# Optimization experiments

Hardware: AMD Instinct MI355X
Metric: run time of the kernel (lower is better)

The kernel has to match this reference:

```python
import jax, jax.numpy as jnp
import numpy as np

N = 100000      # nodes
E = 1600000     # edges (avg degree 16)
F_IN = 128
F_OUT = 128
EPS = 1e-5      # BatchNorm eps


def setup_inputs() -> dict:
    key = jax.random.key(0)
    ks = jax.random.split(key, 10)
    s_in = 1.0 / np.sqrt(F_IN)
    s_out = 1.0 / np.sqrt(F_OUT)
    return {
        "x": jax.random.normal(ks[0], (N, F_IN), dtype=jnp.float32),
        "edge_index": jax.random.randint(ks[1], (2, E), 0, N, dtype=jnp.int32),
        # layer 0: SAGEConv(F_IN, F_OUT, aggr='max'); lin_l has bias, lin_r does not
        "W0_l": jax.random.normal(ks[2], (F_IN, F_OUT), dtype=jnp.float32) * s_in,
        "b0_l": jnp.zeros((F_OUT,), dtype=jnp.float32),
        "W0_r": jax.random.normal(ks[3], (F_IN, F_OUT), dtype=jnp.float32) * s_in,
        "gamma0": jnp.ones((F_OUT,), dtype=jnp.float32),
        "beta0": jnp.zeros((F_OUT,), dtype=jnp.float32),
        # layer 1: SAGEConv(F_OUT, F_OUT, aggr='max')
        "W1_l": jax.random.normal(ks[4], (F_OUT, F_OUT), dtype=jnp.float32) * s_out,
        "b1_l": jnp.zeros((F_OUT,), dtype=jnp.float32),
        "W1_r": jax.random.normal(ks[5], (F_OUT, F_OUT), dtype=jnp.float32) * s_out,
        "gamma1": jnp.ones((F_OUT,), dtype=jnp.float32),
        "beta1": jnp.zeros((F_OUT,), dtype=jnp.float32),
    }


def _sage_conv_max(x, src, dst, W_l, b_l, W_r):
    # gather source features along edges, scatter-max into destination nodes
    msgs = x[src]                                             # [E, F]
    agg = jax.ops.segment_max(msgs, dst, num_segments=N)      # [N, F], -inf for isolated
    agg = jnp.where(jnp.isfinite(agg), agg, 0.0)              # PyG fills empty segments with 0
    return agg @ W_l + b_l + x @ W_r                          # lin_l(aggr) + lin_r(x)


def _batch_norm(h, gamma, beta):
    mu = jnp.mean(h, axis=0)
    var = jnp.var(h, axis=0)
    return (h - mu) * jax.lax.rsqrt(var + EPS) * gamma + beta


def reference(x, edge_index, W0_l, b0_l, W0_r, gamma0, beta0,
              W1_l, b1_l, W1_r, gamma1, beta1):
    src, dst = edge_index[0], edge_index[1]
    h = _sage_conv_max(x, src, dst, W0_l, b0_l, W0_r)
    h = jax.nn.relu(_batch_norm(h, gamma0, beta0))
    h = _sage_conv_max(h, src, dst, W1_l, b1_l, W1_r)
    h = jax.nn.relu(_batch_norm(h, gamma1, beta1))
    return h
```

## Files before the change

### kernel.cpp

```cpp
#include <hip/hip_runtime.h>
#include <stdint.h>

#define EPS_BN 1e-5f

typedef __attribute__((ext_vector_type(8))) short short8v;
typedef __attribute__((ext_vector_type(4))) float f32x4;

__device__ __forceinline__ unsigned rne_bf16(float f) {
    unsigned u = __float_as_uint(f);
    return (u + 0x7FFFu + ((u >> 16) & 1u)) >> 16;
}

extern "C" __global__ __launch_bounds__(256)
void f32_to_bf16_kernel(const float4* __restrict__ in, uint2* __restrict__ out, long n4) {
    long i = (long)blockIdx.x * 256 + threadIdx.x;
    long stride = (long)gridDim.x * 256;
    for (; i < n4; i += stride) {
        float4 v = in[i];
        uint2 o;
        o.x = rne_bf16(v.x) | (rne_bf16(v.y) << 16);
        o.y = rne_bf16(v.z) | (rne_bf16(v.w) << 16);
        out[i] = o;
    }
}

extern "C" __global__ __launch_bounds__(256)
void wt_prep_kernel(const float* __restrict__ Wl, const float* __restrict__ Wr,
                    unsigned short* __restrict__ Wt) {
    int idx = blockIdx.x * 256 + threadIdx.x;
    int col = idx >> 8, k = idx & 255;
    float v = (k < 128) ? Wl[(size_t)k * 128 + col] : Wr[(size_t)(k - 128) * 128 + col];
    Wt[(size_t)col * 256 + k] = (unsigned short)rne_bf16(v);
}

extern "C" __global__ __launch_bounds__(256)
void init_head_kernel(int* __restrict__ head, int n) {
    int i = blockIdx.x * 256 + threadIdx.x;
    if (i < n) head[i] = -1;
}

extern "C" __global__ __launch_bounds__(256)
void link_kernel(const int* __restrict__ ei, int* __restrict__ head,
                 int* __restrict__ next, int E) {
    int e = blockIdx.x * 256 + threadIdx.x;
    if (e < E) {
        int dst = ei[E + e];
        int old = atomicExch(&head[dst], e);
        next[e] = old;
    }
}

extern "C" __global__ __launch_bounds__(256)
void gather_max_ll16_kernel(const uint2* __restrict__ x16, const int* __restrict__ head,
                            const int* __restrict__ next, const int* __restrict__ ei,
                            uint2* __restrict__ agg16, int Nn) {
    int t = blockIdx.x * 256 + threadIdx.x;
    int node = t >> 5;
    if (node >= Nn) return;
    int lane = t & 31;
    int e = head[node];
    uint2 out;
    if (e >= 0) {
        int src = ei[e];
        int en = next[e];
        uint2 u = x16[(size_t)src * 32 + lane];
        float a0 = __uint_as_float(u.x << 16);
        float a1 = __uint_as_float(u.x & 0xFFFF0000u);
        float a2 = __uint_as_float(u.y << 16);
        float a3 = __uint_as_float(u.y & 0xFFFF0000u);
        while (en >= 0) {
            int s2 = ei[en];
            int en2 = next[en];
            uint2 v = x16[(size_t)s2 * 32 + lane];
            en = en2;
            a0 = fmaxf(a0, __uint_as_float(v.x << 16));
            a1 = fmaxf(a1, __uint_as_float(v.x & 0xFFFF0000u));
            a2 = fmaxf(a2, __uint_as_float(v.y << 16));
            a3 = fmaxf(a3, __uint_as_float(v.y & 0xFFFF0000u));
        }
        out.x = (__float_as_uint(a0) >> 16) | (__float_as_uint(a1) & 0xFFFF0000u);
        out.y = (__float_as_uint(a2) >> 16) | (__float_as_uint(a3) & 0xFFFF0000u);
    } else {
        out.x = 0u; out.y = 0u;
    }
    agg16[(size_t)node * 32 + lane] = out;
}

extern "C" __global__ __launch_bounds__(256)
void gemm_bf16_kernel(const unsigned short* __restrict__ agg16,
                      const unsigned short* __restrict__ xin16,
                      const unsigned short* __restrict__ Wt,
                      const float* __restrict__ bias,
                      float* __restrict__ h, float* __restrict__ stats, int nrows) {
    __shared__ float redS[4][128];
    __shared__ float redQ[4][128];

    const int t = threadIdx.x;
    const int w = t >> 6, l = t & 63;
    const int wm = w >> 1, wn = w & 1;
    const int r16 = l & 15, g = l >> 4;
    const int blockRow = blockIdx.x * 128;
    const int colBase = wn * 64;

    f32x4 acc[4][4];
#pragma unroll
    for (int m = 0; m < 4; ++m)
#pragma unroll
        for (int n = 0; n < 4; ++n) acc[m][n] = (f32x4){0.f, 0.f, 0.f, 0.f};

    const short8v az = {0, 0, 0, 0, 0, 0, 0, 0};

#pragma unroll
    for (int kt = 0; kt < 8; ++kt) {
        const unsigned short* Asrc = (kt < 4) ? agg16 : xin16;
        const int kofs = (kt < 4) ? kt * 32 : kt * 32 - 128;

        short8v b[4];
#pragma unroll
        for (int n = 0; n < 4; ++n) {
            int col = colBase + n * 16 + r16;
            b[n] = *(const short8v*)(Wt + (size_t)col * 256 + kt * 32 + g * 8);
        }
        short8v a[4];
#pragma unroll
        for (int m = 0; m < 4; ++m) {
            int row = blockRow + wm * 64 + m * 16 + r16;
            a[m] = (row < nrows)
                 ? *(const short8v*)(Asrc + (size_t)row * 128 + kofs + g * 8)
                 : az;
        }
#pragma unroll
        for (int m = 0; m < 4; ++m)
#pragma unroll
            for (int n = 0; n < 4; ++n)
                acc[m][n] = __builtin_amdgcn_mfma_f32_16x16x32_bf16(a[m], b[n], acc[m][n], 0, 0, 0);
    }

    for (int i = t; i < 512; i += 256) {
        ((float*)redS)[i] = 0.f;
        ((float*)redQ)[i] = 0.f;
    }
    __syncthreads();

    float bcol[4];
#pragma unroll
    for (int n = 0; n < 4; ++n) bcol[n] = bias[colBase + n * 16 + r16];

    float s4[4] = {0.f, 0.f, 0.f, 0.f};
    float q4[4] = {0.f, 0.f, 0.f, 0.f};
#pragma unroll
    for (int m = 0; m < 4; ++m) {
#pragma unroll
        for (int reg = 0; reg < 4; ++reg) {
            int row = blockRow + wm * 64 + m * 16 + g * 4 + reg;
            if (row < nrows) {
#pragma unroll
                for (int n = 0; n < 4; ++n) {
                    float o = acc[m][n][reg] + bcol[n];
                    h[(size_t)row * 128 + colBase + n * 16 + r16] = o;
                    s4[n] += o;
                    q4[n] += o * o;
                }
            }
        }
    }
#pragma unroll
    for (int n = 0; n < 4; ++n) {
        s4[n] += __shfl_xor(s4[n], 16, 64);
        s4[n] += __shfl_xor(s4[n], 32, 64);
        q4[n] += __shfl_xor(q4[n], 16, 64);
        q4[n] += __shfl_xor(q4[n], 32, 64);
    }
    if (g == 0) {
#pragma unroll
        for (int n = 0; n < 4; ++n) {
            redS[w][colBase + n * 16 + r16] = s4[n];
            redQ[w][colBase + n * 16 + r16] = q4[n];
        }
    }
    __syncthreads();
    if (t < 128) {
        float s = redS[0][t] + redS[1][t] + redS[2][t] + redS[3][t];
        float q = redQ[0][t] + redQ[1][t] + redQ[2][t] + redQ[3][t];
        atomicAdd(&stats[t], s);
        atomicAdd(&stats[128 + t], q);
    }
}

extern "C" __global__
void zero_stats_kernel(float* __restrict__ stats) {
    stats[threadIdx.x] = 0.0f;
}

extern "C" __global__
void finalize_kernel(const float* __restrict__ stats, const float* __restrict__ gamma,
                     const float* __restrict__ beta, float* __restrict__ ss, float inv_n) {
    int c = threadIdx.x;
    if (c < 128) {
        float mu = stats[c] * inv_n;
        float var = stats[128 + c] * inv_n - mu * mu;
        float sc = gamma[c] * rsqrtf(var + EPS_BN);
        ss[c] = sc;
        ss[128 + c] = beta[c] - mu * sc;
    }
}

extern "C" __global__ __launch_bounds__(256)
void bn_relu_tobf16_kernel(const float4* __restrict__ h, const float* __restrict__ ss,
                           uint2* __restrict__ y16, long n4) {
    __shared__ float s_ss[256];
    if (threadIdx.x < 256) s_ss[threadIdx.x] = ss[threadIdx.x];
    __syncthreads();
    long i = (long)blockIdx.x * blockDim.x + threadIdx.x;
    long stride = (long)gridDim.x * blockDim.x;
    for (; i < n4; i += stride) {
        int c4 = (int)(i & 31) * 4;
        float4 v = h[i];
        float o0 = fmaxf(fmaf(v.x, s_ss[c4 + 0], s_ss[128 + c4 + 0]), 0.f);
        float o1 = fmaxf(fmaf(v.y, s_ss[c4 + 1], s_ss[128 + c4 + 1]), 0.f);
        float o2 = fmaxf(fmaf(v.z, s_ss[c4 + 2], s_ss[128 + c4 + 2]), 0.f);
        float o3 = fmaxf(fmaf(v.w, s_ss[c4 + 3], s_ss[128 + c4 + 3]), 0.f);
        uint2 o;
        o.x = rne_bf16(o0) | (rne_bf16(o1) << 16);
        o.y = rne_bf16(o2) | (rne_bf16(o3) << 16);
        y16[i] = o;
    }
}

extern "C" __global__ __launch_bounds__(256)
void bn_relu_kernel(float4* __restrict__ h, const float* __restrict__ ss, long n4) {
    __shared__ float s_ss[256];
    if (threadIdx.x < 256) s_ss[threadIdx.x] = ss[threadIdx.x];
    __syncthreads();
    long i = (long)blockIdx.x * blockDim.x + threadIdx.x;
    long stride = (long)gridDim.x * blockDim.x;
    for (; i < n4; i += stride) {
        int c4 = (int)(i & 31) * 4;
        float4 v = h[i];
        v.x = fmaxf(fmaf(v.x, s_ss[c4 + 0], s_ss[128 + c4 + 0]), 0.f);
        v.y = fmaxf(fmaf(v.y, s_ss[c4 + 1], s_ss[128 + c4 + 1]), 0.f);
        v.z = fmaxf(fmaf(v.z, s_ss[c4 + 2], s_ss[128 + c4 + 2]), 0.f);
        v.w = fmaxf(fmaf(v.w, s_ss[c4 + 3], s_ss[128 + c4 + 3]), 0.f);
        h[i] = v;
    }
}

__device__ __forceinline__ unsigned map_f(float f) {
    unsigned u = __float_as_uint(f);
    return (u & 0x80000000u) ? ~u : (u | 0x80000000u);
}
__device__ __forceinline__ float unmap_f(unsigned m) {
    return (m & 0x80000000u) ? __uint_as_float(m & 0x7FFFFFFFu) : __uint_as_float(~m);
}

extern "C" __global__ __launch_bounds__(256)
void init_sentinel_kernel(uint4* __restrict__ agg, long n4) {
    uint4 z = {0u, 0u, 0u, 0u};
    long i = (long)blockIdx.x * blockDim.x + threadIdx.x;
    long stride = (long)gridDim.x * blockDim.x;
    for (; i < n4; i += stride) agg[i] = z;
}

extern "C" __global__ __launch_bounds__(256)
void scatter_max_kernel(const float4* __restrict__ xin, const int* __restrict__ ei,
                        unsigned* __restrict__ agg, int E) {
    int t = blockIdx.x * 256 + threadIdx.x;
    int e = t >> 5;
    if (e >= E) return;
    int f4 = t & 31;
    int src = ei[e];
    int dst = ei[E + e];
    float4 v = xin[(size_t)src * 32 + f4];
    unsigned* p = agg + (size_t)dst * 128 + (size_t)f4 * 4;
    atomicMax(p + 0, map_f(v.x));
    atomicMax(p + 1, map_f(v.y));
    atomicMax(p + 2, map_f(v.z));
    atomicMax(p + 3, map_f(v.w));
}

extern "C" __global__ __launch_bounds__(256)
void unmap_kernel(unsigned* __restrict__ agg, long n) {
    long i = (long)blockIdx.x * blockDim.x + threadIdx.x;
    long stride = (long)gridDim.x * blockDim.x;
    for (; i < n; i += stride) {
        unsigned u = agg[i];
        agg[i] = __float_as_uint(u ? unmap_f(u) : 0.0f);
    }
}

extern "C" __global__ __launch_bounds__(256)
void gemm_kernel(const float* __restrict__ agg, const float* __restrict__ xin,
                 const float* __restrict__ Wl, const float* __restrict__ Wr,
                 const float* __restrict__ bias, float* __restrict__ h,
                 float* __restrict__ stats, int nrows) {
    __shared__ __align__(16) float As[64][36];
    __shared__ __align__(16) float Bs[32][136];
    __shared__ float redS[4][128];
    __shared__ float redQ[4][128];

    const int t = threadIdx.x;
    const int tx = t & 15;
    const int ty = t >> 4;
    const int tx8 = tx * 8;
    const int ty4 = ty * 4;
    const int blockRow = blockIdx.x * 64;

    float acc[4][8];
#pragma unroll
    for (int j = 0; j < 4; ++j)
#pragma unroll
        for (int c = 0; c < 8; ++c) acc[j][c] = 0.0f;

    for (int kt = 0; kt < 8; ++kt) {
        const int k0 = kt * 32;
        const bool isAgg = (kt < 4);
        const float* W = isAgg ? Wl : Wr;
        const float* Asrc = isAgg ? agg : xin;
        const int kw = isAgg ? k0 : (k0 - 128);

#pragma unroll
        for (int it = 0; it < 4; ++it) {
            int idx = t + it * 256;
            int kr = idx >> 5, cq = idx & 31;
            float4 ww = *(const float4*)&W[(size_t)(kw + kr) * 128 + cq * 4];
            *(float4*)&Bs[kr][cq * 4] = ww;
        }
#pragma unroll
        for (int it = 0; it < 2; ++it) {
            int idx = t + it * 256;
            int r = idx >> 3, kq = idx & 7;
            int row_g = blockRow + r;
            float4 a = {0.f, 0.f, 0.f, 0.f};
            if (row_g < nrows)
                a = *(const float4*)&Asrc[(size_t)row_g * 128 + kw + kq * 4];
            *(float4*)&As[r][kq * 4] = a;
        }
        __syncthreads();

#pragma unroll
        for (int kk = 0; kk < 32; ++kk) {
            float aa[4];
            aa[0] = As[ty4 + 0][kk];
            aa[1] = As[ty4 + 1][kk];
            aa[2] = As[ty4 + 2][kk];
            aa[3] = As[ty4 + 3][kk];
            float4 b0 = *(const float4*)&Bs[kk][tx8];
            float4 b1 = *(const float4*)&Bs[kk][tx8 + 4];
            float bb[8] = {b0.x, b0.y, b0.z, b0.w, b1.x, b1.y, b1.z, b1.w};
#pragma unroll
            for (int j = 0; j < 4; ++j)
#pragma unroll
                for (int c = 0; c < 8; ++c)
                    acc[j][c] = fmaf(aa[j], bb[c], acc[j][c]);
        }
        __syncthreads();
    }

    float bv[8];
#pragma unroll
    for (int c = 0; c < 8; ++c) bv[c] = bias[tx8 + c];

    float s_loc[8], q_loc[8];
#pragma unroll
    for (int c = 0; c < 8; ++c) { s_loc[c] = 0.f; q_loc[c] = 0.f; }

#pragma unroll
    for (int j = 0; j < 4; ++j) {
        int row = blockRow + ty4 + j;
        if (row < nrows) {
            float o[8];
#pragma unroll
            for (int c = 0; c < 8; ++c) {
                o[c] = acc[j][c] + bv[c];
                s_loc[c] += o[c];
                q_loc[c] += o[c] * o[c];
            }
            float4 o0 = {o[0], o[1], o[2], o[3]};
            float4 o1 = {o[4], o[5], o[6], o[7]};
            *(float4*)&h[(size_t)row * 128 + tx8] = o0;
            *(float4*)&h[(size_t)row * 128 + tx8 + 4] = o1;
        }
    }

#pragma unroll
    for (int c = 0; c < 8; ++c) {
        s_loc[c] += __shfl_xor(s_loc[c], 16, 64);
        s_loc[c] += __shfl_xor(s_loc[c], 32, 64);
        q_loc[c] += __shfl_xor(q_loc[c], 16, 64);
        q_loc[c] += __shfl_xor(q_loc[c], 32, 64);
    }
    int wave = t >> 6;
    if ((t & 63) < 16) {
#pragma unroll
        for (int c = 0; c < 8; ++c) {
            redS[wave][tx8 + c] = s_loc[c];
            redQ[wave][tx8 + c] = q_loc[c];
        }
    }
    __syncthreads();
    if (t < 128) {
        float s = redS[0][t] + redS[1][t] + redS[2][t] + redS[3][t];
        float q = redQ[0][t] + redQ[1][t] + redQ[2][t] + redQ[3][t];
        atomicAdd(&stats[t], s);
        atomicAdd(&stats[128 + t], q);
    }
}

static void run_layer_bf16(const unsigned short* in16, const int* head, const int* next,
                           const int* ei, int Nn,
                           const unsigned short* Wt, const float* bl,
                           const float* gamma, const float* beta,
                           unsigned short* agg16, float* stats, float* ss,
                           float* h, hipStream_t stream) {
    zero_stats_kernel<<<1, 256, 0, stream>>>(stats);
    gather_max_ll16_kernel<<<(Nn * 32 + 255) / 256, 256, 0, stream>>>(
        (const uint2*)in16, head, next, ei, (uint2*)agg16, Nn);
    gemm_bf16_kernel<<<(Nn + 127) / 128, 256, 0, stream>>>(agg16, in16, Wt, bl,
                                                           h, stats, Nn);
    finalize_kernel<<<1, 128, 0, stream>>>(stats, gamma, beta, ss, 1.0f / (float)Nn);
}

static void run_layer_atomic(const float* in_feat, const int* ei, int Nn, int Ee,
                             const float* Wl, const float* bl, const float* Wr,
                             const float* gamma, const float* beta,
                             float* agg, float* stats, float* ss,
                             float* out, hipStream_t stream) {
    long aggN = (long)Nn * 128;
    long n4 = aggN / 4;

    zero_stats_kernel<<<1, 256, 0, stream>>>(stats);
    int initBlocks = (int)((n4 + 255) / 256);
    if (initBlocks > 4096) initBlocks = 4096;
    init_sentinel_kernel<<<initBlocks, 256, 0, stream>>>((uint4*)agg, n4);
    int sb = (int)(((long)Ee * 32 + 255) / 256);
    scatter_max_kernel<<<sb, 256, 0, stream>>>((const float4*)in_feat, ei,
                                               (unsigned*)agg, Ee);
    int ub = (int)((aggN + 255) / 256);
    if (ub > 8192) ub = 8192;
    unmap_kernel<<<ub, 256, 0, stream>>>((unsigned*)agg, aggN);
    gemm_kernel<<<(Nn + 63) / 64, 256, 0, stream>>>(agg, in_feat, Wl, Wr, bl,
                                                    out, stats, Nn);
    finalize_kernel<<<1, 128, 0, stream>>>(stats, gamma, beta, ss, 1.0f / (float)Nn);
    int bnBlocks = (int)((n4 + 255) / 256);
    if (bnBlocks > 8192) bnBlocks = 8192;
    bn_relu_kernel<<<bnBlocks, 256, 0, stream>>>((float4*)out, ss, n4);
}

extern "C" void kernel_launch(void* const* d_in, const int* in_sizes, int n_in,
                              void* d_out, int out_size, void* d_ws, size_t ws_size,
                              hipStream_t stream) {
    (void)n_in; (void)out_size;
    const float* x     = (const float*)d_in[0];
    const int*   ei    = (const int*)d_in[1];
    const float* W0_l  = (const float*)d_in[2];
    const float* b0_l  = (const float*)d_in[3];
    const float* W0_r  = (const float*)d_in[4];
    const float* g0    = (const float*)d_in[5];
    const float* be0   = (const float*)d_in[6];
    const float* W1_l  = (const float*)d_in[7];
    const float* b1_l  = (const float*)d_in[8];
    const float* W1_r  = (const float*)d_in[9];
    const float* g1    = (const float*)d_in[10];
    const float* be1   = (const float*)d_in[11];

    int Nn = in_sizes[0] / 128;
    int Ee = in_sizes[1] / 2;
    long n4 = (long)Nn * 32;

    char* p = (char*)d_ws;
    unsigned short* xy16 = (unsigned short*)p;  p += (size_t)Nn * 128 * 2;
    unsigned short* agg16 = (unsigned short*)p; p += (size_t)Nn * 128 * 2;
    float* stats = (float*)p;                   p += 256 * sizeof(float);
    float* ss = (float*)p;                      p += 256 * sizeof(float);
    unsigned short* Wt0 = (unsigned short*)p;   p += 128 * 256 * 2;
    unsigned short* Wt1 = (unsigned short*)p;   p += 128 * 256 * 2;
    int* head = (int*)p;                        p += (size_t)Nn * sizeof(int);
    int* next = (int*)p;                        p += (size_t)Ee * sizeof(int);
    size_t needed = (size_t)(p - (char*)d_ws);
    float* out = (float*)d_out;

    if (ws_size >= needed) {
        int cvB = (int)((n4 + 255) / 256);
        if (cvB > 4096) cvB = 4096;
        f32_to_bf16_kernel<<<cvB, 256, 0, stream>>>((const float4*)x, (uint2*)xy16, n4);
        wt_prep_kernel<<<128, 256, 0, stream>>>(W0_l, W0_r, Wt0);
        wt_prep_kernel<<<128, 256, 0, stream>>>(W1_l, W1_r, Wt1);
        init_head_kernel<<<(Nn + 255) / 256, 256, 0, stream>>>(head, Nn);
        link_kernel<<<(Ee + 255) / 256, 256, 0, stream>>>(ei, head, next, Ee);

        run_layer_bf16(xy16, head, next, ei, Nn, Wt0, b0_l, g0, be0,
                       agg16, stats, ss, out, stream);
        int bnB = (int)((n4 + 255) / 256);
        if (bnB > 8192) bnB = 8192;
        bn_relu_tobf16_kernel<<<bnB, 256, 0, stream>>>((const float4*)out, ss,
                                                       (uint2*)xy16, n4);
        run_layer_bf16(xy16, head, next, ei, Nn, Wt1, b1_l, g1, be1,
                       agg16, stats, ss, out, stream);
        bn_relu_kernel<<<bnB, 256, 0, stream>>>((float4*)out, ss, n4);
    } else {
        float* agg = (float*)d_ws;
        float* fstats = (float*)((char*)d_ws + (size_t)Nn * 128 * sizeof(float));
        float* fss = fstats + 256;
        run_layer_atomic(x, ei, Nn, Ee, W0_l, b0_l, W0_r, g0, be0,
                         agg, fstats, fss, out, stream);
        run_layer_atomic(out, ei, Nn, Ee, W1_l, b1_l, W1_r, g1, be1,
                         agg, fstats, fss, out, stream);
    }
}
```

Baseline: 464.0 us.

## Pack src/next edge pairs, widen gather to 16B per lane, fuse stats zeroing

```diff
diff --git a/kernel.cpp b/kernel.cpp
--- a/kernel.cpp
+++ b/kernel.cpp
@@ -41,49 +41,57 @@
 
 extern "C" __global__ __launch_bounds__(256)
 void link_kernel(const int* __restrict__ ei, int* __restrict__ head,
-                 int* __restrict__ next, int E) {
+                 uint2* __restrict__ pair, int E) {
     int e = blockIdx.x * 256 + threadIdx.x;
     if (e < E) {
+        int src = ei[e];
         int dst = ei[E + e];
         int old = atomicExch(&head[dst], e);
-        next[e] = old;
-    }
-}
-
-extern "C" __global__ __launch_bounds__(256)
-void gather_max_ll16_kernel(const uint2* __restrict__ x16, const int* __restrict__ head,
-                            const int* __restrict__ next, const int* __restrict__ ei,
-                            uint2* __restrict__ agg16, int Nn) {
+        uint2 p; p.x = (unsigned)src; p.y = (unsigned)old;
+        pair[e] = p;
+    }
+}
+
+extern "C" __global__ __launch_bounds__(256, 8)
+void gather_max_ll16_kernel(const uint4* __restrict__ x16r, const int* __restrict__ head,
+                            const uint2* __restrict__ pair,
+                            uint4* __restrict__ agg16, float* __restrict__ stats, int Nn) {
+    if (blockIdx.x == 0 && threadIdx.x < 256) stats[threadIdx.x] = 0.0f;
     int t = blockIdx.x * 256 + threadIdx.x;
-    int node = t >> 5;
+    int node = t >> 4;
     if (node >= Nn) return;
-    int lane = t & 31;
+    int lane = t & 15;
     int e = head[node];
-    uint2 out;
+    uint4 out;
     if (e >= 0) {
-        int src = ei[e];
-        int en = next[e];
-        uint2 u = x16[(size_t)src * 32 + lane];
-        float a0 = __uint_as_float(u.x << 16);
-        float a1 = __uint_as_float(u.x & 0xFFFF0000u);
-        float a2 = __uint_as_float(u.y << 16);
-        float a3 = __uint_as_float(u.y & 0xFFFF0000u);
+        uint2 p = pair[e];
+        uint4 r = x16r[(size_t)p.x * 16 + lane];
+        float a0 = __uint_as_float(r.x << 16), a1 = __uint_as_float(r.x);
+        float a2 = __uint_as_float(r.y << 16), a3 = __uint_as_float(r.y);
+        float a4 = __uint_as_float(r.z << 16), a5 = __uint_as_float(r.z);
+        float a6 = __uint_as_float(r.w << 16), a7 = __uint_as_float(r.w);
+        int en = (int)p.y;
         while (en >= 0) {
-            int s2 = ei[en];
-            int en2 = next[en];
-            uint2 v = x16[(size_t)s2 * 32 + lane];
-            en = en2;
+            uint2 pn = pair[en];
+            uint4 v = x16r[(size_t)pn.x * 16 + lane];
+            en = (int)pn.y;
             a0 = fmaxf(a0, __uint_as_float(v.x << 16));
-            a1 = fmaxf(a1, __uint_as_float(v.x & 0xFFFF0000u));
+            a1 = fmaxf(a1, __uint_as_float(v.x));
             a2 = fmaxf(a2, __uint_as_float(v.y << 16));
-            a3 = fmaxf(a3, __uint_as_float(v.y & 0xFFFF0000u));
+            a3 = fmaxf(a3, __uint_as_float(v.y));
+            a4 = fmaxf(a4, __uint_as_float(v.z << 16));
+            a5 = fmaxf(a5, __uint_as_float(v.z));
+            a6 = fmaxf(a6, __uint_as_float(v.w << 16));
+            a7 = fmaxf(a7, __uint_as_float(v.w));
         }
         out.x = (__float_as_uint(a0) >> 16) | (__float_as_uint(a1) & 0xFFFF0000u);
         out.y = (__float_as_uint(a2) >> 16) | (__float_as_uint(a3) & 0xFFFF0000u);
+        out.z = (__float_as_uint(a4) >> 16) | (__float_as_uint(a5) & 0xFFFF0000u);
+        out.w = (__float_as_uint(a6) >> 16) | (__float_as_uint(a7) & 0xFFFF0000u);
     } else {
-        out.x = 0u; out.y = 0u;
-    }
-    agg16[(size_t)node * 32 + lane] = out;
+        out.x = out.y = out.z = out.w = 0u;
+    }
+    agg16[(size_t)node * 16 + lane] = out;
 }
 
 extern "C" __global__ __launch_bounds__(256)
@@ -406,15 +414,13 @@
     }
 }
 
-static void run_layer_bf16(const unsigned short* in16, const int* head, const int* next,
-                           const int* ei, int Nn,
-                           const unsigned short* Wt, const float* bl,
+static void run_layer_bf16(const unsigned short* in16, const int* head, const uint2* pair,
+                           int Nn, const unsigned short* Wt, const float* bl,
                            const float* gamma, const float* beta,
                            unsigned short* agg16, float* stats, float* ss,
                            float* h, hipStream_t stream) {
-    zero_stats_kernel<<<1, 256, 0, stream>>>(stats);
-    gather_max_ll16_kernel<<<(Nn * 32 + 255) / 256, 256, 0, stream>>>(
-        (const uint2*)in16, head, next, ei, (uint2*)agg16, Nn);
+    gather_max_ll16_kernel<<<(Nn * 16 + 255) / 256, 256, 0, stream>>>(
+        (const uint4*)in16, head, pair, (uint4*)agg16, stats, Nn);
     gemm_bf16_kernel<<<(Nn + 127) / 128, 256, 0, stream>>>(agg16, in16, Wt, bl,
                                                            h, stats, Nn);
     finalize_kernel<<<1, 128, 0, stream>>>(stats, gamma, beta, ss, 1.0f / (float)Nn);
@@ -475,7 +481,7 @@
     unsigned short* Wt0 = (unsigned short*)p;   p += 128 * 256 * 2;
     unsigned short* Wt1 = (unsigned short*)p;   p += 128 * 256 * 2;
     int* head = (int*)p;                        p += (size_t)Nn * sizeof(int);
-    int* next = (int*)p;                        p += (size_t)Ee * sizeof(int);
+    uint2* pair = (uint2*)p;                    p += (size_t)Ee * sizeof(uint2);
     size_t needed = (size_t)(p - (char*)d_ws);
     float* out = (float*)d_out;
 
@@ -486,15 +492,15 @@
         wt_prep_kernel<<<128, 256, 0, stream>>>(W0_l, W0_r, Wt0);
         wt_prep_kernel<<<128, 256, 0, stream>>>(W1_l, W1_r, Wt1);
         init_head_kernel<<<(Nn + 255) / 256, 256, 0, stream>>>(head, Nn);
-        link_kernel<<<(Ee + 255) / 256, 256, 0, stream>>>(ei, head, next, Ee);
-
-        run_layer_bf16(xy16, head, next, ei, Nn, Wt0, b0_l, g0, be0,
+        link_kernel<<<(Ee + 255) / 256, 256, 0, stream>>>(ei, head, pair, Ee);
+
+        run_layer_bf16(xy16, head, pair, Nn, Wt0, b0_l, g0, be0,
                        agg16, stats, ss, out, stream);
         int bnB = (int)((n4 + 255) / 256);
         if (bnB > 8192) bnB = 8192;
         bn_relu_tobf16_kernel<<<bnB, 256, 0, stream>>>((const float4*)out, ss,
                                                        (uint2*)xy16, n4);
-        run_layer_bf16(xy16, head, next, ei, Nn, Wt1, b1_l, g1, be1,
+        run_layer_bf16(xy16, head, pair, Nn, Wt1, b1_l, g1, be1,
                        agg16, stats, ss, out, stream);
         bn_relu_kernel<<<bnB, 256, 0, stream>>>((float4*)out, ss, n4);
     } else {
```

New measurement: 405.8 us. -12.5%, faster.
